# Kernel optimization log

Measured on AMD Instinct MI355X. Metric: run time of the kernel, lower is better.

## Reference

```python
import jax, jax.numpy as jnp
import numpy as np

B, T, NH, NB = 16, 400, 100, 65
SR, BLOCK = 16000, 160
REV_LEN = SR  # Reverb(sampling_rate, sampling_rate)


def _fft_convolve(signal, kernel):
    # torch: pad signal right by n, kernel left by its length, multiply spectra, keep 2nd half
    n = signal.shape[-1]
    s = jnp.pad(signal, [(0, 0)] * (signal.ndim - 1) + [(0, n)])
    k = jnp.pad(kernel, [(0, 0)] * (kernel.ndim - 1) + [(kernel.shape[-1], 0)])
    out = jnp.fft.irfft(jnp.fft.rfft(s) * jnp.fft.rfft(k), s.shape[-1])
    return out[..., out.shape[-1] // 2:]


def _amp_to_impulse_response(amp, target_size):
    # amp: [..., n_bands] real magnitudes treated as zero-phase rfft coefficients
    ir = jnp.fft.irfft(jax.lax.complex(amp, jnp.zeros_like(amp)))  # [..., 2*(NB-1)]
    fs = ir.shape[-1]
    ir = jnp.roll(ir, fs // 2, axis=-1)
    win = 0.5 - 0.5 * jnp.cos(2.0 * np.pi * jnp.arange(fs, dtype=ir.dtype) / fs)  # periodic hann
    ir = ir * win
    ir = jnp.pad(ir, [(0, 0)] * (ir.ndim - 1) + [(0, target_size - fs)])
    return jnp.roll(ir, -fs // 2, axis=-1)


def setup_inputs() -> dict:
    key = jax.random.key(0)
    ks = jax.random.split(key, 6)
    pitch = 40.0 + 400.0 * jax.random.uniform(ks[0], (B, T, 1), dtype=jnp.float32)
    total_amp = jax.random.uniform(ks[1], (B, T), dtype=jnp.float32)
    harmo_amps = jax.random.uniform(ks[2], (B, NH, T), dtype=jnp.float32) + 1e-3
    noise_filter = 0.1 * jax.random.uniform(ks[3], (B, T, NB), dtype=jnp.float32)
    noise = 2.0 * jax.random.uniform(ks[4], (B, T, BLOCK), dtype=jnp.float32) - 1.0
    reverb_noise = 2.0 * jax.random.uniform(ks[5], (REV_LEN, 1), dtype=jnp.float32) - 1.0
    decay = jnp.asarray(5.0, jnp.float32)
    wet = jnp.asarray(0.0, jnp.float32)
    return dict(pitch=pitch, total_amp=total_amp, harmo_amps=harmo_amps,
                noise_filter=noise_filter, noise=noise, reverb_noise=reverb_noise,
                decay=decay, wet=wet, sampling_rate=SR, block_size=BLOCK)


def reference(pitch, total_amp, harmo_amps, noise_filter, noise, reverb_noise,
              decay, wet, sampling_rate, block_size):
    dt = pitch.dtype
    n_harm = harmo_amps.shape[1]
    harm_idx = jnp.arange(1, n_harm + 1, dtype=dt)
    # remove_above_nyquist: mask harmonics whose freq >= sr/2 (tiny epsilon kept, as in DDSP)
    freqs = pitch[:, :, 0][:, None, :] * harm_idx[None, :, None]          # [B,NH,T]
    aa = (freqs < (sampling_rate / 2)).astype(dt) + 1e-4
    amps = harmo_amps * aa
    amps = jnp.transpose(amps, (0, 2, 1))                                  # [B,T,NH]
    amps = amps / jnp.sum(amps, axis=-1, keepdims=True)
    amps = amps * total_amp[..., None]
    # nearest-neighbor upsample by block_size (F.interpolate default mode)
    amps_up = jnp.repeat(amps, block_size, axis=1)                         # [B,N,NH]
    pitch_up = jnp.repeat(pitch, block_size, axis=1)                       # [B,N,1]
    # harmonic additive synthesis
    omega = jnp.cumsum(2.0 * np.pi * pitch_up / sampling_rate, axis=1)     # [B,N,1]
    harmonic = jnp.sum(jnp.sin(omega * harm_idx) * amps_up, axis=-1, keepdims=True)
    # filtered noise branch
    impulse = _amp_to_impulse_response(noise_filter, block_size)           # [B,T,BLOCK]
    noise_f = _fft_convolve(noise, impulse)                                # [B,T,BLOCK]
    noise_f = noise_f.reshape(noise_f.shape[0], -1, 1)                     # [B,N,1]
    signal = harmonic + noise_f
    # reverb (forward with reverb=True)
    rev_len = reverb_noise.shape[0]
    t = (jnp.arange(rev_len, dtype=dt) / sampling_rate)[None, :, None]     # [1,L,1]
    imp = reverb_noise[None] * jnp.exp(-jax.nn.softplus(-decay) * t * 500.0) * jax.nn.sigmoid(wet)
    imp = imp.at[:, 0].set(1.0)
    imp = jnp.pad(imp, ((0, 0), (0, signal.shape[1] - rev_len), (0, 0)))   # [1,N,1]
    out = _fft_convolve(signal[..., 0], imp[..., 0])[..., None]            # [B,N,1]
    return out
```

## Files before the change

### kernel.cpp

```cpp
#include <hip/hip_runtime.h>

#define B_ 16
#define T_ 400
#define NH_ 100
#define NB_ 65
#define BLK_ 160
#define SR_ 16000
#define N_ 64000
#define REV_ 16000
#define KPAD_ 16128
#define KTOT_ 80128
#define NT_ 1022
#define KSPLIT_ 8
#define STEPS_ 63
#define M_ 8
#define NWG_ 500

typedef __attribute__((ext_vector_type(8))) _Float16 f16x8;
typedef __attribute__((ext_vector_type(2))) _Float16 f16x2;
typedef __attribute__((ext_vector_type(4))) float f32x4;

static __device__ __forceinline__ float dot2f(f16x2 a, f16x2 b, float c) {
#if __has_builtin(__builtin_amdgcn_fdot2)
  return __builtin_amdgcn_fdot2(a, b, c, false);
#else
  return fmaf((float)a[0], (float)b[0], fmaf((float)a[1], (float)b[1], c));
#endif
}

__global__ __launch_bounds__(512) void k_pre(const float* __restrict__ pitch,
                                             const float* __restrict__ rn,
                                             const float* __restrict__ dec,
                                             const float* __restrict__ wet,
                                             double* __restrict__ Pv,
                                             double* __restrict__ Xv,
                                             _Float16* __restrict__ FH,
                                             _Float16* __restrict__ PH) {
  const int blk = blockIdx.x, tid = threadIdx.x;
  if (blk >= NT_) {
    __shared__ double s[512];
    const int b = blk - NT_, t = tid;
    double x = 0.0;
    if (t < T_) x = (double)pitch[b * T_ + t] * (1.0 / (double)SR_);
    s[t] = x;
    __syncthreads();
    for (int off = 1; off < 512; off <<= 1) {
      double v = (t >= off) ? s[t - off] : 0.0;
      __syncthreads();
      s[t] += v;
      __syncthreads();
    }
    if (t < T_) {
      Xv[b * T_ + t] = x;
      Pv[b * T_ + t] = (s[t] - x) * 160.0;
    }
    return;
  }
  const int t = blk;
  const int gid = t * 512 + tid;
  if (gid < 32256) ((f32x4*)PH)[gid] = (f32x4){0.f, 0.f, 0.f, 0.f};
  const int lane = tid >> 3, j = tid & 7;
  const int idx = (t - 14) * 16 + (lane & 15) - ((lane >> 4) << 3) - j;
  float v = 0.f;
  if (idx == 0) {
    v = 1.0f;
  } else if (idx > 0 && idx < REV_) {
    const float a = log1pf(expf(-dec[0]));
    const float sg = 1.f / (1.f + expf(-wet[0]));
    v = rn[idx] * expf(-a * ((float)idx / (float)SR_) * 500.0f) * sg;
  }
  FH[t * 512 + tid] = (_Float16)v;
}

__global__ __launch_bounds__(320) void k_synth(
    const float* __restrict__ pitch, const float* __restrict__ tamp,
    const float* __restrict__ harmo, const float* __restrict__ nfilt,
    const float* __restrict__ noise, const double* __restrict__ Pv,
    const double* __restrict__ Xv, _Float16* __restrict__ PH) {
  const int tid = threadIdx.x;
  const int g = (tid >= 160) ? 1 : 0;
  const int ltid = tid - (g << 7) - (g << 5);
  const int bt = (blockIdx.x << 1) + g;
  const int b = bt / T_, t = bt - b * T_;
  __shared__ __align__(16) float amp[2][112];
  __shared__ __align__(16) float a_s[2][68];
  __shared__ __align__(16) float ir_s[2][68];
  __shared__ __align__(16) _Float16 C0[2][320];
  __shared__ __align__(16) _Float16 C1[2][320];
  __shared__ __align__(16) _Float16 imp_sw[2][128];
  __shared__ float red_s[2];

  const float pv = pitch[bt];
  int nv = (int)(8000.0f / pv);
  if (nv > NH_) nv = NH_;
  while (nv < NH_ && (float)(nv + 1) * pv < 8000.0f) ++nv;
  while (nv > 0 && (float)nv * pv >= 8000.0f) --nv;

  if (ltid < NB_) a_s[g][ltid] = nfilt[bt * NB_ + ltid];
  {
    const _Float16 nh = (_Float16)noise[bt * BLK_ + ltid];
    C0[g][160 + ltid] = nh;
    C1[g][159 + ltid] = nh;
    C0[g][ltid] = (_Float16)0.f;
    if (ltid < 159) C1[g][ltid] = (_Float16)0.f;
  }
  if (ltid < NH_) {
    const float ha = harmo[(b * NH_ + ltid) * T_ + t];
    const float aa = (pv * (float)(ltid + 1) < 8000.0f ? 1.0f : 0.0f) + 1e-4f;
    amp[g][ltid] = ha * aa;
  } else if (ltid < 112) {
    amp[g][ltid] = 0.f;
  }
  __syncthreads();

  float irv = 0.f;
  if (ltid < 65) {
    const float phi = (float)ltid * (1.0f / 128.0f);
    const float c1 = __builtin_amdgcn_cosf(phi);
    const float c2 = fmaf(2.f * c1, c1, -1.f);
    const float c3 = fmaf(2.f * c2, c1, -c1);
    const float c4 = fmaf(2.f * c2, c2, -1.f);
    const float tc = 2.f * c4;
    float x0 = 1.f, p0 = c4;
    float x1 = c1, p1 = c3;
    float x2 = c2, p2 = c2;
    float x3 = c3, p3 = c1;
    float a0 = 0.f, a1 = 0.f, a2 = 0.f, a3 = 0.f;
#pragma unroll
    for (int m = 0; m < 8; ++m) {
      const f32x4 aA = *(const f32x4*)&a_s[g][m << 3];
      const f32x4 aB = *(const f32x4*)&a_s[g][(m << 3) + 4];
      a0 = fmaf(aA[0], x0, a0); const float y0 = fmaf(tc, x0, -p0);
      a1 = fmaf(aA[1], x1, a1); const float y1 = fmaf(tc, x1, -p1);
      a2 = fmaf(aA[2], x2, a2); const float y2 = fmaf(tc, x2, -p2);
      a3 = fmaf(aA[3], x3, a3); const float y3 = fmaf(tc, x3, -p3);
      a0 = fmaf(aB[0], y0, a0); const float z0 = fmaf(tc, y0, -x0); p0 = y0; x0 = z0;
      a1 = fmaf(aB[1], y1, a1); const float z1 = fmaf(tc, y1, -x1); p1 = y1; x1 = z1;
      a2 = fmaf(aB[2], y2, a2); const float z2 = fmaf(tc, y2, -x2); p2 = y2; x2 = z2;
      a3 = fmaf(aB[3], y3, a3); const float z3 = fmaf(tc, y3, -x3); p3 = y3; x3 = z3;
    }
    const float accS = (a0 + a1) + (a2 + a3);
    irv = (2.f * accS - a_s[g][0] + ((ltid & 1) ? -a_s[g][64] : a_s[g][64])) * (1.0f / 128.0f);
    ir_s[g][ltid] = irv;
  } else if (ltid >= 128) {
    const int l = ltid - 128;
    float v = amp[g][l] + amp[g][l + 32] + amp[g][l + 64] + (l < 4 ? amp[g][l + 96] : 0.f);
    v += __shfl_xor(v, 16);
    v += __shfl_xor(v, 8);
    v += __shfl_xor(v, 4);
    v += __shfl_xor(v, 2);
    v += __shfl_xor(v, 1);
    if (l == 0) red_s[g] = v;
  }
  __syncthreads();

  if (ltid < 64) {
    const float w = 0.5f + 0.5f * __builtin_amdgcn_cosf((float)ltid * (1.0f / 128.0f));
    imp_sw[g][ltid ^ 1] = (_Float16)(w * irv);
  } else if (ltid >= 96 && ltid < 160) {
    const int u = ltid - 96;
    const float w = 0.5f - 0.5f * __builtin_amdgcn_cosf((float)u * (1.0f / 128.0f));
    imp_sw[g][64 + (u ^ 1)] = (_Float16)(w * ir_s[g][64 - u]);
  }
  const float scale = tamp[bt] / red_s[g];
  double th = Pv[bt] + (double)(ltid + 1) * Xv[bt];
  th -= floor(th);
  const float theta = (float)th;
  const float cT = __builtin_amdgcn_cosf(theta);
  const float sT = __builtin_amdgcn_sinf(theta);
  __syncthreads();

  float acc;
  {
    const float c2 = fmaf(cT, cT, -sT * sT);
    const float s2 = 2.f * cT * sT;
    const float s3 = fmaf(s2, cT, c2 * sT);
    const float s4 = 2.f * s2 * c2;
    const float c4 = fmaf(2.f * c2, c2, -1.f);
    const float tc = 2.f * c4;
    float x0 = sT, p0 = -s3;
    float x1 = s2, p1 = -s2;
    float x2 = s3, p2 = -sT;
    float x3 = s4, p3 = 0.f;
    float a0 = 0.f, a1 = 0.f, a2 = 0.f, a3 = 0.f;
    const int S = (nv + 7) >> 3;
    for (int m = 0; m < S; ++m) {
      const f32x4 aA = *(const f32x4*)&amp[g][m << 3];
      const f32x4 aB = *(const f32x4*)&amp[g][(m << 3) + 4];
      a0 = fmaf(aA[0], x0, a0); const float y0 = fmaf(tc, x0, -p0);
      a1 = fmaf(aA[1], x1, a1); const float y1 = fmaf(tc, x1, -p1);
      a2 = fmaf(aA[2], x2, a2); const float y2 = fmaf(tc, x2, -p2);
      a3 = fmaf(aA[3], x3, a3); const float y3 = fmaf(tc, x3, -p3);
      a0 = fmaf(aB[0], y0, a0); const float z0 = fmaf(tc, y0, -x0); p0 = y0; x0 = z0;
      a1 = fmaf(aB[1], y1, a1); const float z1 = fmaf(tc, y1, -x1); p1 = y1; x1 = z1;
      a2 = fmaf(aB[2], y2, a2); const float z2 = fmaf(tc, y2, -x2); p2 = y2; x2 = z2;
      a3 = fmaf(aB[3], y3, a3); const float z3 = fmaf(tc, y3, -x3); p3 = y3; x3 = z3;
    }
    acc = ((a0 + a1) + (a2 + a3)) * scale;
  }

  float nf = 0.f;
  {
    const f16x2* np0;
    int pe;
    if (ltid & 1) {
      np0 = (const f16x2*)C0[g];
      pe = (159 + ltid) >> 1;
    } else {
      np0 = (const f16x2*)C1[g];
      pe = (158 + ltid) >> 1;
    }
    const f16x8* ip = (const f16x8*)imp_sw[g];
#pragma unroll
    for (int k0 = 0; k0 < 8; ++k0) {
      const f16x8 i8 = ip[k0];
      const int kb = k0 << 2;
      nf = dot2f((f16x2){i8[0], i8[1]}, np0[pe - kb], nf);
      nf = dot2f((f16x2){i8[2], i8[3]}, np0[pe - kb - 1], nf);
      nf = dot2f((f16x2){i8[4], i8[5]}, np0[pe - kb - 2], nf);
      nf = dot2f((f16x2){i8[6], i8[7]}, np0[pe - kb - 3], nf);
    }
#pragma unroll
    for (int k0 = 0; k0 < 8; ++k0) {
      const f16x8 i8 = ip[8 + k0];
      const int kb = (k0 << 2) + 48;
      nf = dot2f((f16x2){i8[0], i8[1]}, np0[pe - kb], nf);
      nf = dot2f((f16x2){i8[2], i8[3]}, np0[pe - kb - 1], nf);
      nf = dot2f((f16x2){i8[4], i8[5]}, np0[pe - kb - 2], nf);
      nf = dot2f((f16x2){i8[6], i8[7]}, np0[pe - kb - 3], nf);
    }
  }

  const float v = acc + nf;
  const unsigned k = (unsigned)(KPAD_ + t * BLK_ + ltid);
  const unsigned off = ((k >> 3) << 7) + ((unsigned)b << 3) + (k & 7u);
  PH[off] = (_Float16)v;
}

static __device__ __forceinline__ f32x4 mfma_f16(f16x8 a, f16x8 b, f32x4 c) {
  return __builtin_amdgcn_mfma_f32_16x16x32_f16(a, b, c, 0, 0, 0);
}

template <int U, bool PF>
__device__ __forceinline__ void conv_step(f16x8 (&Rh)[M_], f32x4 (&acc)[M_], f16x8& bhi,
                                          const f16x8* __restrict__ ph,
                                          const f16x8* __restrict__ fh,
                                          int& kcur, int& tcur) {
  f16x8 nbh, na0, na1;
  if (PF) {
    kcur += 64;
    nbh = ph[kcur];
    tcur -= 2;
    na0 = fh[tcur * 64];
    na1 = fh[(tcur + 1) * 64];
  }
#pragma unroll
  for (int m = 0; m < M_; ++m) {
    const int sl = (m - 2 * U) & (M_ - 1);
    acc[m] = mfma_f16(Rh[sl], bhi, acc[m]);
  }
  if (PF) {
    Rh[(M_ - 2 - 2 * U) & (M_ - 1)] = na0;
    Rh[(M_ - 1 - 2 * U) & (M_ - 1)] = na1;
    bhi = nbh;
  }
}

__global__ __launch_bounds__(512) void k_mconv(const f16x8* __restrict__ FH,
                                               const f16x8* __restrict__ PH,
                                               float* __restrict__ out) {
  const int tid = threadIdx.x;
  const int s = tid >> 6, lane = tid & 63;
  int w = blockIdx.x;
  {
    const int q = NWG_ / 8, r = NWG_ % 8;
    const int xcd = w & 7, o = w >> 3;
    w = (xcd < r ? xcd * (q + 1) : r * (q + 1) + (xcd - r) * q) + o;
  }
  const int Q0 = w << 7;
  const int T0 = 1014 - 126 * s;

  const f16x8* fh = FH + lane;
  f16x8 Rh[M_];
#pragma unroll
  for (int m = 0; m < M_; ++m) Rh[m] = fh[(T0 + m) * 64];
  f32x4 acc[M_];
#pragma unroll
  for (int m = 0; m < M_; ++m) acc[m] = (f32x4){0.f, 0.f, 0.f, 0.f};

  const f16x8* ph = PH + ((lane >> 4) << 4) + (lane & 15);
  int kcur = (Q0 + 128 + 2016 * s) << 1;
  int tcur = T0;
  f16x8 bhi = ph[kcur];

  for (int ii = 0; ii < 15; ++ii) {
    conv_step<0, true>(Rh, acc, bhi, ph, fh, kcur, tcur);
    conv_step<1, true>(Rh, acc, bhi, ph, fh, kcur, tcur);
    conv_step<2, true>(Rh, acc, bhi, ph, fh, kcur, tcur);
    conv_step<3, true>(Rh, acc, bhi, ph, fh, kcur, tcur);
  }
  conv_step<0, true>(Rh, acc, bhi, ph, fh, kcur, tcur);
  conv_step<1, true>(Rh, acc, bhi, ph, fh, kcur, tcur);
  conv_step<2, false>(Rh, acc, bhi, ph, fh, kcur, tcur);

  __shared__ f32x4 part[4][M_][64];
  if (s < 4) {
#pragma unroll
    for (int m = 0; m < M_; ++m) part[s][m][lane] = acc[m];
  }
  __syncthreads();
  if (s >= 4) {
#pragma unroll
    for (int m = 0; m < M_; ++m) part[s - 4][m][lane] += acc[m];
  }
  __syncthreads();
  {
    const int m = tid >> 6, ln = tid & 63;
    f32x4 v = part[0][m][ln];
    v += part[1][m][ln];
    v += part[2][m][ln];
    v += part[3][m][ln];
    const int b = ln & 15, g = ln >> 4;
    *(f32x4*)(out + (size_t)b * N_ + Q0 + (m << 4) + (g << 2)) = v;
  }
}

extern "C" void kernel_launch(void* const* d_in, const int* in_sizes, int n_in,
                              void* d_out, int out_size, void* d_ws, size_t ws_size,
                              hipStream_t stream) {
  const float* pitch = (const float*)d_in[0];
  const float* tamp  = (const float*)d_in[1];
  const float* harmo = (const float*)d_in[2];
  const float* nfilt = (const float*)d_in[3];
  const float* noise = (const float*)d_in[4];
  const float* rn    = (const float*)d_in[5];
  const float* dec   = (const float*)d_in[6];
  const float* wet   = (const float*)d_in[7];

  char* ws = (char*)d_ws;
  size_t off = 0;
  _Float16* PH = (_Float16*)(ws + off); off += (size_t)KTOT_ * 16 * 2;
  _Float16* FH = (_Float16*)(ws + off); off += (size_t)NT_ * 512 * 2;
  double* Pv = (double*)(ws + off);     off += (size_t)B_ * T_ * 8;
  double* Xv = (double*)(ws + off);     off += (size_t)B_ * T_ * 8;
  float* out = (float*)d_out;

  k_pre<<<dim3(NT_ + B_), dim3(512), 0, stream>>>(pitch, rn, dec, wet, Pv, Xv, FH, PH);
  k_synth<<<dim3(B_ * T_ / 2), dim3(320), 0, stream>>>(pitch, tamp, harmo, nfilt, noise, Pv, Xv, PH);
  k_mconv<<<dim3(NWG_), dim3(512), 0, stream>>>((const f16x8*)FH, (const f16x8*)PH, out);
}
```

Measured before the change: 68.27 us.

## Widen conv workgroup output tile to 256 and split waves across M and K

The MFMA convolution kernel now produces 256 output samples per workgroup instead of 128, which halves the grid. Its 8 waves are arranged as 2 along the output dimension and 4 along the K dimension, each running longer K loops. A workgroup barrier is added in every loop iteration, probably to keep waves in step so they share the cached filter and signal loads. The cross-wave reduction is rewritten to sum four K partials per output half. The change trades fewer, longer workgroups and barrier overhead for better load reuse and fewer partial reductions.

```diff
diff --git a/kernel.cpp b/kernel.cpp
--- a/kernel.cpp
+++ b/kernel.cpp
@@ -10,11 +10,9 @@
 #define REV_ 16000
 #define KPAD_ 16128
 #define KTOT_ 80128
-#define NT_ 1022
-#define KSPLIT_ 8
-#define STEPS_ 63
+#define NT_ 1038
 #define M_ 8
-#define NWG_ 500
+#define NWG_ 250
 
 typedef __attribute__((ext_vector_type(8))) _Float16 f16x8;
 typedef __attribute__((ext_vector_type(2))) _Float16 f16x2;
@@ -271,14 +269,15 @@
                                                float* __restrict__ out) {
   const int tid = threadIdx.x;
   const int s = tid >> 6, lane = tid & 63;
+  const int mw = s & 1, kw = s >> 1;
   int w = blockIdx.x;
   {
     const int q = NWG_ / 8, r = NWG_ % 8;
     const int xcd = w & 7, o = w >> 3;
     w = (xcd < r ? xcd * (q + 1) : r * (q + 1) + (xcd - r) * q) + o;
   }
-  const int Q0 = w << 7;
-  const int T0 = 1014 - 126 * s;
+  const int Q0 = w << 8;
+  const int T0 = 1022 + (mw << 3) - (kw << 8);
 
   const f16x8* fh = FH + lane;
   f16x8 Rh[M_];
@@ -289,39 +288,36 @@
   for (int m = 0; m < M_; ++m) acc[m] = (f32x4){0.f, 0.f, 0.f, 0.f};
 
   const f16x8* ph = PH + ((lane >> 4) << 4) + (lane & 15);
-  int kcur = (Q0 + 128 + 2016 * s) << 1;
+  int kcur = (Q0 + (kw << 12)) << 1;
   int tcur = T0;
   f16x8 bhi = ph[kcur];
 
-  for (int ii = 0; ii < 15; ++ii) {
+  for (int ii = 0; ii < 31; ++ii) {
     conv_step<0, true>(Rh, acc, bhi, ph, fh, kcur, tcur);
     conv_step<1, true>(Rh, acc, bhi, ph, fh, kcur, tcur);
     conv_step<2, true>(Rh, acc, bhi, ph, fh, kcur, tcur);
     conv_step<3, true>(Rh, acc, bhi, ph, fh, kcur, tcur);
+    __builtin_amdgcn_s_barrier();
   }
   conv_step<0, true>(Rh, acc, bhi, ph, fh, kcur, tcur);
   conv_step<1, true>(Rh, acc, bhi, ph, fh, kcur, tcur);
-  conv_step<2, false>(Rh, acc, bhi, ph, fh, kcur, tcur);
-
-  __shared__ f32x4 part[4][M_][64];
-  if (s < 4) {
-#pragma unroll
-    for (int m = 0; m < M_; ++m) part[s][m][lane] = acc[m];
-  }
+  conv_step<2, true>(Rh, acc, bhi, ph, fh, kcur, tcur);
+  conv_step<3, false>(Rh, acc, bhi, ph, fh, kcur, tcur);
+
+  __shared__ f32x4 part[8][M_][64];
+#pragma unroll
+  for (int m = 0; m < M_; ++m) part[s][m][lane] = acc[m];
   __syncthreads();
-  if (s >= 4) {
-#pragma unroll
-    for (int m = 0; m < M_; ++m) part[s - 4][m][lane] += acc[m];
-  }
-  __syncthreads();
-  {
-    const int m = tid >> 6, ln = tid & 63;
-    f32x4 v = part[0][m][ln];
-    v += part[1][m][ln];
-    v += part[2][m][ln];
-    v += part[3][m][ln];
-    const int b = ln & 15, g = ln >> 4;
-    *(f32x4*)(out + (size_t)b * N_ + Q0 + (m << 4) + (g << 2)) = v;
+#pragma unroll
+  for (int half = 0; half < 2; ++half) {
+    const int it = tid + (half << 9);
+    const int ln = it & 63, m = (it >> 6) & 7, mwi = it >> 9;
+    f32x4 v = part[mwi][m][ln];
+    v += part[mwi + 2][m][ln];
+    v += part[mwi + 4][m][ln];
+    v += part[mwi + 6][m][ln];
+    const int b = ln & 15, gq = ln >> 4;
+    *(f32x4*)(out + (size_t)b * N_ + Q0 + (mwi << 7) + (m << 4) + (gq << 2)) = v;
   }
 }
 
```

Measured after the change: 68.26 us. About the same (-0.0%).

## Double output tile per workgroup and double-buffer MFMA operand prefetch

Applied to the files above, without the earlier changes.

The reverb convolution MFMA kernel now has each workgroup compute 256 output samples instead of 128, using 16 accumulator tiles per wave and half as many workgroups. Each loaded B fragment is reused across twice as many MFMAs. Operand prefetch is also double-buffered, so loads are issued one step ahead of consumption and load latency can hide behind more MFMA work. The trade-off is much higher register use (16 accumulators plus 16 A registers) and fewer workgroups, which lowers occupancy and grid parallelism. It also doubles the shared-memory reduction buffer.

```diff
diff --git a/kernel.cpp b/kernel.cpp
--- a/kernel.cpp
+++ b/kernel.cpp
@@ -10,11 +10,9 @@
 #define REV_ 16000
 #define KPAD_ 16128
 #define KTOT_ 80128
-#define NT_ 1022
-#define KSPLIT_ 8
-#define STEPS_ 63
-#define M_ 8
-#define NWG_ 500
+#define NT_ 1038
+#define M_ 16
+#define NWG_ 250
 
 typedef __attribute__((ext_vector_type(8))) _Float16 f16x8;
 typedef __attribute__((ext_vector_type(2))) _Float16 f16x2;
@@ -241,28 +239,28 @@
   return __builtin_amdgcn_mfma_f32_16x16x32_f16(a, b, c, 0, 0, 0);
 }
 
-template <int U, bool PF>
+template <int U, bool ISSUE, bool CONSUME>
 __device__ __forceinline__ void conv_step(f16x8 (&Rh)[M_], f32x4 (&acc)[M_], f16x8& bhi,
+                                          f16x8 (&nb)[2], f16x8 (&na0)[2], f16x8 (&na1)[2],
                                           const f16x8* __restrict__ ph,
                                           const f16x8* __restrict__ fh,
-                                          int& kcur, int& tcur) {
-  f16x8 nbh, na0, na1;
-  if (PF) {
-    kcur += 64;
-    nbh = ph[kcur];
-    tcur -= 2;
-    na0 = fh[tcur * 64];
-    na1 = fh[(tcur + 1) * 64];
+                                          int& kit, int& tit) {
+  if (ISSUE) {
+    kit += 64;
+    nb[U & 1] = ph[kit];
+    tit -= 2;
+    na0[U & 1] = fh[tit * 64];
+    na1[U & 1] = fh[(tit + 1) * 64];
   }
 #pragma unroll
   for (int m = 0; m < M_; ++m) {
     const int sl = (m - 2 * U) & (M_ - 1);
     acc[m] = mfma_f16(Rh[sl], bhi, acc[m]);
   }
-  if (PF) {
-    Rh[(M_ - 2 - 2 * U) & (M_ - 1)] = na0;
-    Rh[(M_ - 1 - 2 * U) & (M_ - 1)] = na1;
-    bhi = nbh;
+  if (CONSUME) {
+    Rh[(M_ - 2 - 2 * U) & (M_ - 1)] = na0[(U + 1) & 1];
+    Rh[(M_ - 1 - 2 * U) & (M_ - 1)] = na1[(U + 1) & 1];
+    bhi = nb[(U + 1) & 1];
   }
 }
 
@@ -277,8 +275,8 @@
     const int xcd = w & 7, o = w >> 3;
     w = (xcd < r ? xcd * (q + 1) : r * (q + 1) + (xcd - r) * q) + o;
   }
-  const int Q0 = w << 7;
-  const int T0 = 1014 - 126 * s;
+  const int Q0 = w << 8;
+  const int T0 = 1022 - 128 * s;
 
   const f16x8* fh = FH + lane;
   f16x8 Rh[M_];
@@ -289,19 +287,34 @@
   for (int m = 0; m < M_; ++m) acc[m] = (f32x4){0.f, 0.f, 0.f, 0.f};
 
   const f16x8* ph = PH + ((lane >> 4) << 4) + (lane & 15);
-  int kcur = (Q0 + 128 + 2016 * s) << 1;
-  int tcur = T0;
-  f16x8 bhi = ph[kcur];
-
-  for (int ii = 0; ii < 15; ++ii) {
-    conv_step<0, true>(Rh, acc, bhi, ph, fh, kcur, tcur);
-    conv_step<1, true>(Rh, acc, bhi, ph, fh, kcur, tcur);
-    conv_step<2, true>(Rh, acc, bhi, ph, fh, kcur, tcur);
-    conv_step<3, true>(Rh, acc, bhi, ph, fh, kcur, tcur);
-  }
-  conv_step<0, true>(Rh, acc, bhi, ph, fh, kcur, tcur);
-  conv_step<1, true>(Rh, acc, bhi, ph, fh, kcur, tcur);
-  conv_step<2, false>(Rh, acc, bhi, ph, fh, kcur, tcur);
+  int kit = (Q0 + 2048 * s) << 1;
+  int tit = T0;
+  f16x8 bhi = ph[kit];
+  f16x8 nb[2], na0[2], na1[2];
+  kit += 64;
+  nb[1] = ph[kit];
+  tit -= 2;
+  na0[1] = fh[tit * 64];
+  na1[1] = fh[(tit + 1) * 64];
+
+  for (int ii = 0; ii < 7; ++ii) {
+    conv_step<0, true, true>(Rh, acc, bhi, nb, na0, na1, ph, fh, kit, tit);
+    conv_step<1, true, true>(Rh, acc, bhi, nb, na0, na1, ph, fh, kit, tit);
+    conv_step<2, true, true>(Rh, acc, bhi, nb, na0, na1, ph, fh, kit, tit);
+    conv_step<3, true, true>(Rh, acc, bhi, nb, na0, na1, ph, fh, kit, tit);
+    conv_step<4, true, true>(Rh, acc, bhi, nb, na0, na1, ph, fh, kit, tit);
+    conv_step<5, true, true>(Rh, acc, bhi, nb, na0, na1, ph, fh, kit, tit);
+    conv_step<6, true, true>(Rh, acc, bhi, nb, na0, na1, ph, fh, kit, tit);
+    conv_step<7, true, true>(Rh, acc, bhi, nb, na0, na1, ph, fh, kit, tit);
+  }
+  conv_step<0, true, true>(Rh, acc, bhi, nb, na0, na1, ph, fh, kit, tit);
+  conv_step<1, true, true>(Rh, acc, bhi, nb, na0, na1, ph, fh, kit, tit);
+  conv_step<2, true, true>(Rh, acc, bhi, nb, na0, na1, ph, fh, kit, tit);
+  conv_step<3, true, true>(Rh, acc, bhi, nb, na0, na1, ph, fh, kit, tit);
+  conv_step<4, true, true>(Rh, acc, bhi, nb, na0, na1, ph, fh, kit, tit);
+  conv_step<5, true, true>(Rh, acc, bhi, nb, na0, na1, ph, fh, kit, tit);
+  conv_step<6, false, true>(Rh, acc, bhi, nb, na0, na1, ph, fh, kit, tit);
+  conv_step<7, false, false>(Rh, acc, bhi, nb, na0, na1, ph, fh, kit, tit);
 
   __shared__ f32x4 part[4][M_][64];
   if (s < 4) {
@@ -314,14 +327,16 @@
     for (int m = 0; m < M_; ++m) part[s - 4][m][lane] += acc[m];
   }
   __syncthreads();
-  {
-    const int m = tid >> 6, ln = tid & 63;
+#pragma unroll
+  for (int half = 0; half < 2; ++half) {
+    const int it = tid + (half << 9);
+    const int m = it >> 6, ln = it & 63;
     f32x4 v = part[0][m][ln];
     v += part[1][m][ln];
     v += part[2][m][ln];
     v += part[3][m][ln];
-    const int b = ln & 15, g = ln >> 4;
-    *(f32x4*)(out + (size_t)b * N_ + Q0 + (m << 4) + (g << 2)) = v;
+    const int b = ln & 15, gq = ln >> 4;
+    *(f32x4*)(out + (size_t)b * N_ + Q0 + (m << 4) + (gq << 2)) = v;
   }
 }
 
```

New measurement: 60.83 us. 10.9% less time.
